# Optimization experiments

Hardware: AMD Instinct MI355X
Metric: run time of the kernel (lower is better)

Reference implementation:

```python
import jax, jax.numpy as jnp
import numpy as np

B, C, H, W, O = 32, 512, 28, 28, 1024


def _make_sketch(key, input_dim, output_dim):
    kh, ks = jax.random.split(key)
    rand_h = jax.random.randint(kh, (input_dim,), 0, output_dim)
    rand_s = jax.random.randint(ks, (input_dim,), 0, 2).astype(jnp.float32) * 2.0 - 1.0
    sketch = jnp.zeros((output_dim, input_dim), dtype=jnp.float32)
    return sketch.at[rand_h, jnp.arange(input_dim)].set(rand_s)


def setup_inputs() -> dict:
    key = jax.random.key(0)
    k1, k2, k3, k4 = jax.random.split(key, 4)
    x1 = jax.random.normal(k1, (B, C, H, W), dtype=jnp.float32)
    x2 = jax.random.normal(k2, (B, C, H, W), dtype=jnp.float32)
    sketch1 = _make_sketch(k3, C, O)
    sketch2 = _make_sketch(k4, C, O)
    return {"x1": x1, "x2": x2, "sketch1": sketch1, "sketch2": sketch2}


def reference(x1, x2, sketch1, sketch2):
    b, c, h, w = x1.shape
    out_dim = sketch1.shape[0]
    # [B, C, H*W] -> [B, N, C]
    x1_flat = x1.reshape(b, c, h * w).transpose(0, 2, 1)
    x2_flat = x2.reshape(b, c, h * w).transpose(0, 2, 1)
    # count-sketch projection via dense matmul (faithful to F.linear)
    proj1 = jnp.einsum('bnc,oc->bno', x1_flat, sketch1)
    proj2 = jnp.einsum('bnc,oc->bno', x2_flat, sketch2)
    orig_dtype = proj1.dtype
    # circular convolution via FFT along output_dim axis
    fft1 = jnp.fft.fft(proj1.astype(jnp.float32), axis=-1)
    fft2 = jnp.fft.fft(proj2.astype(jnp.float32), axis=-1)
    cbp_flat = jnp.fft.ifft(fft1 * fft2, axis=-1).real.astype(orig_dtype)
    # [B, N, O] -> [B, O, H, W]
    return cbp_flat.transpose(0, 2, 1).reshape(b, out_dim, h, w)
```

## Files before the change

### kernel.cpp

```cpp
#include <hip/hip_runtime.h>

#define O_DIM   1024
#define C_DIM   512
#define HW      784
#define B_DIM   32
#define T_POS   8
#define NTILES  (HW / T_POS)
#define NTHREADS 256

__device__ __forceinline__ float2 cmul(float2 a, float2 b) {
    return make_float2(a.x * b.x - a.y * b.y, a.x * b.y + a.y * b.x);
}

template<int SGN>
__device__ __forceinline__ void fft32(float2 y[32]) {
    static constexpr float C32[16] = {
        1.f, 0.98078528f, 0.92387953f, 0.83146961f,
        0.70710678f, 0.55557023f, 0.38268343f, 0.19509032f,
        0.f, -0.19509032f, -0.38268343f, -0.55557023f,
        -0.70710678f, -0.83146961f, -0.92387953f, -0.98078528f};
    static constexpr float S32[16] = {
        0.f, 0.19509032f, 0.38268343f, 0.55557023f,
        0.70710678f, 0.83146961f, 0.92387953f, 0.98078528f,
        1.f, 0.98078528f, 0.92387953f, 0.83146961f,
        0.70710678f, 0.55557023f, 0.38268343f, 0.19509032f};
#pragma unroll
    for (int s = 0; s < 5; ++s) {
        const int L = 32 >> s;
        const int h = 16 >> s;
#pragma unroll
        for (int u = 0; u < 16; ++u) {
            const int blk = u >> (4 - s);
            const int t   = u & (h - 1);
            const int i   = blk * L + t;
            const int m   = t << s;
            float2 a = y[i], b = y[i + h];
            y[i] = make_float2(a.x + b.x, a.y + b.y);
            float2 d = make_float2(a.x - b.x, a.y - b.y);
            if (m == 0) {
                y[i + h] = d;
            } else if (m == 8) {
                y[i + h] = (SGN < 0) ? make_float2(d.y, -d.x)
                                     : make_float2(-d.y, d.x);
            } else {
                float2 w = make_float2(C32[m], (SGN < 0) ? -S32[m] : S32[m]);
                y[i + h] = cmul(d, w);
            }
        }
    }
}

__device__ const int REV5[32] = {
    0,16,8,24,4,20,12,28,2,18,10,26,6,22,14,30,
    1,17,9,25,5,21,13,29,3,19,11,27,7,23,15,31};

template<int SGN>
__device__ __forceinline__ void four_step_core(float2* zg, int p, float2 y[32]) {
#pragma unroll
    for (int n2 = 0; n2 < 32; ++n2)
        y[n2] = zg[p + 32 * n2];
    __builtin_amdgcn_wave_barrier();
    fft32<SGN>(y);
    float sv, cv;
    __sincosf((float)SGN * 6.283185307179586f * (float)p * (1.f / 1024.f), &sv, &cv);
    const float2 stw = make_float2(cv, sv);
    float2 w = make_float2(1.f, 0.f);
#pragma unroll
    for (int k2 = 0; k2 < 32; ++k2) {
        float2 val = y[REV5[k2]];
        if (k2 > 0) val = cmul(val, w);
        zg[k2 * 32 + ((p + k2) & 31)] = val;
        w = cmul(w, stw);
    }
    __builtin_amdgcn_wave_barrier();
#pragma unroll
    for (int n1 = 0; n1 < 32; ++n1)
        y[n1] = zg[p * 32 + ((n1 + p) & 31)];
    __builtin_amdgcn_wave_barrier();
    fft32<SGN>(y);
}

__global__ void extract_sketch(const float* __restrict__ sk1,
                               const float* __restrict__ sk2,
                               int* __restrict__ h, float* __restrict__ s) {
    const int o = blockIdx.x;
    for (int c = threadIdx.x; c < C_DIM; c += blockDim.x) {
        float v1 = sk1[o * C_DIM + c];
        if (v1 != 0.f) { h[c] = o; s[c] = v1; }
        float v2 = sk2[o * C_DIM + c];
        if (v2 != 0.f) { h[C_DIM + c] = o; s[C_DIM + c] = v2; }
    }
}

__global__ __launch_bounds__(NTHREADS, 2)
void cbp_main(const float* __restrict__ x1, const float* __restrict__ x2,
              const int* __restrict__ h1, const int* __restrict__ h2,
              const float* __restrict__ s1, const float* __restrict__ s2,
              float* __restrict__ out) {
    __shared__ float4 LBUF[4096];
    float2 (*Z)[O_DIM] = reinterpret_cast<float2(*)[O_DIM]>(LBUF);
    float*  R = reinterpret_cast<float*>(LBUF);

    const int tid  = threadIdx.x;
    const int b    = blockIdx.x / NTILES;
    const int tile = blockIdx.x % NTILES;
    const int n0   = tile * T_POS;

    const int c0 = tid;
    const int c1 = tid + NTHREADS;
    const int xoff = b * (C_DIM * HW) + n0;
    const float4* p10 = (const float4*)(x1 + xoff + c0 * HW);
    const float4* p11 = (const float4*)(x1 + xoff + c1 * HW);
    const float4* p20 = (const float4*)(x2 + xoff + c0 * HW);
    const float4* p21 = (const float4*)(x2 + xoff + c1 * HW);
    float4 a0 = p10[0], a1 = p10[1];
    float4 b0 = p11[0], b1 = p11[1];
    float4 d0 = p20[0], d1 = p20[1];
    float4 e0 = p21[0], e1 = p21[1];
    const int   q10 = h1[c0], q11 = h1[c1], q20 = h2[c0], q21 = h2[c1];
    const float w10 = s1[c0], w11 = s1[c1], w20 = s2[c0], w21 = s2[c1];

#pragma unroll
    for (int i = 0; i < 4096 / NTHREADS; ++i)
        LBUF[tid + NTHREADS * i] = make_float4(0.f, 0.f, 0.f, 0.f);
    __syncthreads();

    {
        float v[8];
        v[0]=a0.x; v[1]=a0.y; v[2]=a0.z; v[3]=a0.w;
        v[4]=a1.x; v[5]=a1.y; v[6]=a1.z; v[7]=a1.w;
#pragma unroll
        for (int j = 0; j < 8; ++j) atomicAdd(&Z[j][q10].x, w10 * v[j]);
        v[0]=b0.x; v[1]=b0.y; v[2]=b0.z; v[3]=b0.w;
        v[4]=b1.x; v[5]=b1.y; v[6]=b1.z; v[7]=b1.w;
#pragma unroll
        for (int j = 0; j < 8; ++j) atomicAdd(&Z[j][q11].x, w11 * v[j]);
        v[0]=d0.x; v[1]=d0.y; v[2]=d0.z; v[3]=d0.w;
        v[4]=d1.x; v[5]=d1.y; v[6]=d1.z; v[7]=d1.w;
#pragma unroll
        for (int j = 0; j < 8; ++j) atomicAdd(&Z[j][q20].y, w20 * v[j]);
        v[0]=e0.x; v[1]=e0.y; v[2]=e0.z; v[3]=e0.w;
        v[4]=e1.x; v[5]=e1.y; v[6]=e1.z; v[7]=e1.w;
#pragma unroll
        for (int j = 0; j < 8; ++j) atomicAdd(&Z[j][q21].y, w21 * v[j]);
    }
    __syncthreads();

    const int g = tid >> 5;
    const int p = tid & 31;
    float2* zg = &Z[g][0];
    float2 y[32];

    four_step_core<-1>(zg, p, y);
#pragma unroll
    for (int k1 = 0; k1 < 32; ++k1)
        zg[p + 32 * k1] = y[REV5[k1]];
    __builtin_amdgcn_wave_barrier();

#pragma unroll
    for (int m = 0; m < 16; ++m) {
        const int k = p + (m << 5);
        if (k == 0) {
            float2 z0 = zg[0];
            float2 z5 = zg[512];
            zg[0]   = make_float2(z0.x * z0.y, 0.f);
            zg[512] = make_float2(z5.x * z5.y, 0.f);
        } else {
            float2 za = zg[k];
            float2 zb = zg[1024 - k];
            float2 F1 = make_float2(0.5f * (za.x + zb.x), 0.5f * (za.y - zb.y));
            float2 F2 = make_float2(0.5f * (za.y + zb.y), -0.5f * (za.x - zb.x));
            float2 G  = cmul(F1, F2);
            zg[k]        = G;
            zg[1024 - k] = make_float2(G.x, -G.y);
        }
    }
    __builtin_amdgcn_wave_barrier();

    four_step_core<1>(zg, p, y);
    __syncthreads();

#pragma unroll
    for (int k1 = 0; k1 < 32; ++k1)
        R[(p + 32 * k1) * 10 + g] = y[REV5[k1]].x * (1.f / 1024.f);
    __syncthreads();

    const int obase = b * (O_DIM * HW) + n0;
#pragma unroll
    for (int r = 0; r < O_DIM / NTHREADS; ++r) {
        const int o = tid + NTHREADS * r;
        const float* rp = &R[o * 10];
        float4 v0 = make_float4(rp[0], rp[1], rp[2], rp[3]);
        float4 v1 = make_float4(rp[4], rp[5], rp[6], rp[7]);
        float4* dst = (float4*)(out + obase + o * HW);
        dst[0] = v0;
        dst[1] = v1;
    }
}

extern "C" void kernel_launch(void* const* d_in, const int* in_sizes, int n_in,
                              void* d_out, int out_size, void* d_ws, size_t ws_size,
                              hipStream_t stream) {
    const float* x1  = (const float*)d_in[0];
    const float* x2  = (const float*)d_in[1];
    const float* sk1 = (const float*)d_in[2];
    const float* sk2 = (const float*)d_in[3];
    float* out = (float*)d_out;

    int*   h = (int*)d_ws;
    float* s = (float*)((char*)d_ws + 4096);

    hipLaunchKernelGGL(extract_sketch, dim3(O_DIM), dim3(256), 0, stream,
                       sk1, sk2, h, s);
    hipLaunchKernelGGL(cbp_main, dim3(B_DIM * NTILES), dim3(NTHREADS), 0, stream,
                       x1, x2, h, h + C_DIM, s, s + C_DIM, out);
}
```

Baseline: 363.1 us.

## Split each 1024-point FFT across a full wave using permlane32 swaps

Doubles the block to 512 threads so each 64-lane wave handles one position's 1024-point FFT instead of 32 lanes. The first radix-2 stage of each 32-point sub-FFT is done across wave halves with permlane32_swap, leaving 16 points per lane. This halves per-thread register arrays and spreads the scatter-add over one channel per thread, aiming for higher occupancy (launch bounds raised to 4 blocks). The result staging pad is changed from 10 to 11 to reduce LDS bank conflicts. It adds cross-lane traffic and more LDS contention per CU.

```diff
diff --git a/kernel.cpp b/kernel.cpp
--- a/kernel.cpp
+++ b/kernel.cpp
@@ -6,78 +6,103 @@
 #define B_DIM   32
 #define T_POS   8
 #define NTILES  (HW / T_POS)
-#define NTHREADS 256
+#define NTHREADS 512
+#define RPAD    11
 
 __device__ __forceinline__ float2 cmul(float2 a, float2 b) {
     return make_float2(a.x * b.x - a.y * b.y, a.x * b.y + a.y * b.x);
 }
 
+static constexpr float C32T[16] = {
+    1.f, 0.98078528f, 0.92387953f, 0.83146961f,
+    0.70710678f, 0.55557023f, 0.38268343f, 0.19509032f,
+    0.f, -0.19509032f, -0.38268343f, -0.55557023f,
+    -0.70710678f, -0.83146961f, -0.92387953f, -0.98078528f};
+static constexpr float S32T[16] = {
+    0.f, 0.19509032f, 0.38268343f, 0.55557023f,
+    0.70710678f, 0.83146961f, 0.92387953f, 0.98078528f,
+    1.f, 0.98078528f, 0.92387953f, 0.83146961f,
+    0.70710678f, 0.55557023f, 0.38268343f, 0.19509032f};
+static constexpr int REV4[16] = {0,8,4,12,2,10,6,14,1,9,5,13,3,11,7,15};
+
+__device__ __forceinline__ float other_half(float v) {
+    unsigned u = __float_as_uint(v);
+    auto r = __builtin_amdgcn_permlane32_swap(u, u, false, false);
+    return __uint_as_float(((unsigned)r[0]) ^ ((unsigned)r[1]) ^ u);
+}
+
 template<int SGN>
-__device__ __forceinline__ void fft32(float2 y[32]) {
-    static constexpr float C32[16] = {
-        1.f, 0.98078528f, 0.92387953f, 0.83146961f,
-        0.70710678f, 0.55557023f, 0.38268343f, 0.19509032f,
-        0.f, -0.19509032f, -0.38268343f, -0.55557023f,
-        -0.70710678f, -0.83146961f, -0.92387953f, -0.98078528f};
-    static constexpr float S32[16] = {
-        0.f, 0.19509032f, 0.38268343f, 0.55557023f,
-        0.70710678f, 0.83146961f, 0.92387953f, 0.98078528f,
-        1.f, 0.98078528f, 0.92387953f, 0.83146961f,
-        0.70710678f, 0.55557023f, 0.38268343f, 0.19509032f};
-#pragma unroll
-    for (int s = 0; s < 5; ++s) {
-        const int L = 32 >> s;
-        const int h = 16 >> s;
-#pragma unroll
-        for (int u = 0; u < 16; ++u) {
-            const int blk = u >> (4 - s);
-            const int t   = u & (h - 1);
+__device__ __forceinline__ void fft16x(float2 y[16], int h) {
+#pragma unroll
+    for (int j = 0; j < 16; ++j) {
+        float2 own = y[j];
+        float2 oth = make_float2(other_half(own.x), other_half(own.y));
+        float2 s = make_float2(own.x + oth.x, own.y + oth.y);
+        float2 f = make_float2(own.x - oth.x, own.y - oth.y);
+        float2 dd;
+        if (j == 0) {
+            dd = make_float2(-f.x, -f.y);
+        } else if (j == 8) {
+            dd = (SGN < 0) ? make_float2(-f.y, f.x) : make_float2(f.y, -f.x);
+        } else {
+            float2 wn = make_float2(-C32T[j], (SGN < 0) ? S32T[j] : -S32T[j]);
+            dd = cmul(f, wn);
+        }
+        y[j] = h ? dd : s;
+    }
+#pragma unroll
+    for (int s = 0; s < 4; ++s) {
+        const int hh = 8 >> s;
+        const int L  = 16 >> s;
+#pragma unroll
+        for (int u = 0; u < 8; ++u) {
+            const int blk = u >> (3 - s);
+            const int t   = u & (hh - 1);
             const int i   = blk * L + t;
-            const int m   = t << s;
-            float2 a = y[i], b = y[i + h];
+            const int m   = (t << s) * 2;
+            float2 a = y[i], b = y[i + hh];
             y[i] = make_float2(a.x + b.x, a.y + b.y);
             float2 d = make_float2(a.x - b.x, a.y - b.y);
             if (m == 0) {
-                y[i + h] = d;
+                y[i + hh] = d;
             } else if (m == 8) {
-                y[i + h] = (SGN < 0) ? make_float2(d.y, -d.x)
-                                     : make_float2(-d.y, d.x);
+                y[i + hh] = (SGN < 0) ? make_float2(d.y, -d.x)
+                                      : make_float2(-d.y, d.x);
             } else {
-                float2 w = make_float2(C32[m], (SGN < 0) ? -S32[m] : S32[m]);
-                y[i + h] = cmul(d, w);
+                float2 wv = make_float2(C32T[m], (SGN < 0) ? -S32T[m] : S32T[m]);
+                y[i + hh] = cmul(d, wv);
             }
         }
     }
 }
 
-__device__ const int REV5[32] = {
-    0,16,8,24,4,20,12,28,2,18,10,26,6,22,14,30,
-    1,17,9,25,5,21,13,29,3,19,11,27,7,23,15,31};
-
 template<int SGN>
-__device__ __forceinline__ void four_step_core(float2* zg, int p, float2 y[32]) {
-#pragma unroll
-    for (int n2 = 0; n2 < 32; ++n2)
-        y[n2] = zg[p + 32 * n2];
-    __builtin_amdgcn_wave_barrier();
-    fft32<SGN>(y);
-    float sv, cv;
-    __sincosf((float)SGN * 6.283185307179586f * (float)p * (1.f / 1024.f), &sv, &cv);
-    const float2 stw = make_float2(cv, sv);
-    float2 w = make_float2(1.f, 0.f);
-#pragma unroll
-    for (int k2 = 0; k2 < 32; ++k2) {
-        float2 val = y[REV5[k2]];
-        if (k2 > 0) val = cmul(val, w);
-        zg[k2 * 32 + ((p + k2) & 31)] = val;
+__device__ __forceinline__ void wave_fft(float2* zg, int c, int h, float2 y[16]) {
+#pragma unroll
+    for (int j = 0; j < 16; ++j)
+        y[j] = zg[c + 32 * (16 * h + j)];
+    __builtin_amdgcn_wave_barrier();
+    fft16x<SGN>(y, h);
+    float sv, cv, sv2, cv2;
+    __sincosf((float)SGN * 6.283185307179586f * (float)(c * h) * (1.f / 1024.f),
+              &sv, &cv);
+    __sincosf((float)SGN * 6.283185307179586f * (float)(2 * c) * (1.f / 1024.f),
+              &sv2, &cv2);
+    float2 w = make_float2(cv, sv);
+    const float2 stw = make_float2(cv2, sv2);
+#pragma unroll
+    for (int mm = 0; mm < 16; ++mm) {
+        float2 val = cmul(y[REV4[mm]], w);
+        const int k2 = 2 * mm + h;
+        zg[k2 * 32 + ((c + k2) & 31)] = val;
         w = cmul(w, stw);
     }
     __builtin_amdgcn_wave_barrier();
 #pragma unroll
-    for (int n1 = 0; n1 < 32; ++n1)
-        y[n1] = zg[p * 32 + ((n1 + p) & 31)];
-    __builtin_amdgcn_wave_barrier();
-    fft32<SGN>(y);
+    for (int j = 0; j < 16; ++j)
+        y[j] = zg[c * 32 + ((16 * h + j + c) & 31)];
+    __builtin_amdgcn_wave_barrier();
+    fft16x<SGN>(y, h);
 }
 
 __global__ void extract_sketch(const float* __restrict__ sk1,
@@ -92,7 +117,7 @@
     }
 }
 
-__global__ __launch_bounds__(NTHREADS, 2)
+__global__ __launch_bounds__(NTHREADS, 4)
 void cbp_main(const float* __restrict__ x1, const float* __restrict__ x2,
               const int* __restrict__ h1, const int* __restrict__ h2,
               const float* __restrict__ s1, const float* __restrict__ s2,
@@ -106,19 +131,13 @@
     const int tile = blockIdx.x % NTILES;
     const int n0   = tile * T_POS;
 
-    const int c0 = tid;
-    const int c1 = tid + NTHREADS;
-    const int xoff = b * (C_DIM * HW) + n0;
-    const float4* p10 = (const float4*)(x1 + xoff + c0 * HW);
-    const float4* p11 = (const float4*)(x1 + xoff + c1 * HW);
-    const float4* p20 = (const float4*)(x2 + xoff + c0 * HW);
-    const float4* p21 = (const float4*)(x2 + xoff + c1 * HW);
-    float4 a0 = p10[0], a1 = p10[1];
-    float4 b0 = p11[0], b1 = p11[1];
-    float4 d0 = p20[0], d1 = p20[1];
-    float4 e0 = p21[0], e1 = p21[1];
-    const int   q10 = h1[c0], q11 = h1[c1], q20 = h2[c0], q21 = h2[c1];
-    const float w10 = s1[c0], w11 = s1[c1], w20 = s2[c0], w21 = s2[c1];
+    const int c = tid;
+    const float* px1 = x1 + b * (C_DIM * HW) + c * HW + n0;
+    const float* px2 = x2 + b * (C_DIM * HW) + c * HW + n0;
+    float4 a0 = ((const float4*)px1)[0], a1 = ((const float4*)px1)[1];
+    float4 d0 = ((const float4*)px2)[0], d1 = ((const float4*)px2)[1];
+    const int   q1 = h1[c], q2 = h2[c];
+    const float w1 = s1[c], w2 = s2[c];
 
 #pragma unroll
     for (int i = 0; i < 4096 / NTHREADS; ++i)
@@ -126,40 +145,31 @@
     __syncthreads();
 
     {
-        float v[8];
-        v[0]=a0.x; v[1]=a0.y; v[2]=a0.z; v[3]=a0.w;
-        v[4]=a1.x; v[5]=a1.y; v[6]=a1.z; v[7]=a1.w;
-#pragma unroll
-        for (int j = 0; j < 8; ++j) atomicAdd(&Z[j][q10].x, w10 * v[j]);
-        v[0]=b0.x; v[1]=b0.y; v[2]=b0.z; v[3]=b0.w;
-        v[4]=b1.x; v[5]=b1.y; v[6]=b1.z; v[7]=b1.w;
-#pragma unroll
-        for (int j = 0; j < 8; ++j) atomicAdd(&Z[j][q11].x, w11 * v[j]);
-        v[0]=d0.x; v[1]=d0.y; v[2]=d0.z; v[3]=d0.w;
-        v[4]=d1.x; v[5]=d1.y; v[6]=d1.z; v[7]=d1.w;
-#pragma unroll
-        for (int j = 0; j < 8; ++j) atomicAdd(&Z[j][q20].y, w20 * v[j]);
-        v[0]=e0.x; v[1]=e0.y; v[2]=e0.z; v[3]=e0.w;
-        v[4]=e1.x; v[5]=e1.y; v[6]=e1.z; v[7]=e1.w;
-#pragma unroll
-        for (int j = 0; j < 8; ++j) atomicAdd(&Z[j][q21].y, w21 * v[j]);
-    }
-    __syncthreads();
-
-    const int g = tid >> 5;
-    const int p = tid & 31;
-    float2* zg = &Z[g][0];
-    float2 y[32];
-
-    four_step_core<-1>(zg, p, y);
-#pragma unroll
-    for (int k1 = 0; k1 < 32; ++k1)
-        zg[p + 32 * k1] = y[REV5[k1]];
-    __builtin_amdgcn_wave_barrier();
-
-#pragma unroll
-    for (int m = 0; m < 16; ++m) {
-        const int k = p + (m << 5);
+        float v[8] = {a0.x, a0.y, a0.z, a0.w, a1.x, a1.y, a1.z, a1.w};
+#pragma unroll
+        for (int j = 0; j < 8; ++j) atomicAdd(&Z[j][q1].x, w1 * v[j]);
+        float u[8] = {d0.x, d0.y, d0.z, d0.w, d1.x, d1.y, d1.z, d1.w};
+#pragma unroll
+        for (int j = 0; j < 8; ++j) atomicAdd(&Z[j][q2].y, w2 * u[j]);
+    }
+    __syncthreads();
+
+    const int wv   = tid >> 6;
+    const int lane = tid & 63;
+    const int cc   = lane & 31;
+    const int hh   = lane >> 5;
+    float2* zg = &Z[wv][0];
+    float2 y[16];
+
+    wave_fft<-1>(zg, cc, hh, y);
+#pragma unroll
+    for (int mm = 0; mm < 16; ++mm)
+        zg[cc + 32 * (2 * mm + hh)] = y[REV4[mm]];
+    __builtin_amdgcn_wave_barrier();
+
+#pragma unroll
+    for (int m = 0; m < 8; ++m) {
+        const int k = lane + (m << 6);
         if (k == 0) {
             float2 z0 = zg[0];
             float2 z5 = zg[512];
@@ -177,19 +187,19 @@
     }
     __builtin_amdgcn_wave_barrier();
 
-    four_step_core<1>(zg, p, y);
-    __syncthreads();
-
-#pragma unroll
-    for (int k1 = 0; k1 < 32; ++k1)
-        R[(p + 32 * k1) * 10 + g] = y[REV5[k1]].x * (1.f / 1024.f);
+    wave_fft<1>(zg, cc, hh, y);
+    __syncthreads();
+
+#pragma unroll
+    for (int mm = 0; mm < 16; ++mm)
+        R[(cc + 32 * (2 * mm + hh)) * RPAD + wv] = y[REV4[mm]].x * (1.f / 1024.f);
     __syncthreads();
 
     const int obase = b * (O_DIM * HW) + n0;
 #pragma unroll
     for (int r = 0; r < O_DIM / NTHREADS; ++r) {
         const int o = tid + NTHREADS * r;
-        const float* rp = &R[o * 10];
+        const float* rp = &R[o * RPAD];
         float4 v0 = make_float4(rp[0], rp[1], rp[2], rp[3]);
         float4 v1 = make_float4(rp[4], rp[5], rp[6], rp[7]);
         float4* dst = (float4*)(out + obase + o * HW);
```

Result: slower. 383.6 us (+5.6%).

## Do spectral product in registers via ds_bpermute and split twiddle recurrence

Applied to the files above, without the earlier changes.

After the forward FFT, the spectrum is no longer written back to LDS and re-read for the pointwise product. Each lane instead fetches its mirror element k and 1024-k from the partner lane with ds_bpermute and computes the product in registers, then feeds the result directly into the inverse FFT. The twiddle recurrence is split into four independent chains seeded with stw^8, stw^16 and stw^24, which shortens the dependency chain, and REV5 becomes a constexpr so indexing resolves at compile time. The cost is higher register pressure from the extra gg[32] array, which could hurt occupancy under launch_bounds(256,2).

```diff
diff --git a/kernel.cpp b/kernel.cpp
--- a/kernel.cpp
+++ b/kernel.cpp
@@ -11,6 +11,10 @@
 __device__ __forceinline__ float2 cmul(float2 a, float2 b) {
     return make_float2(a.x * b.x - a.y * b.y, a.x * b.y + a.y * b.x);
 }
+
+static constexpr int REV5[32] = {
+    0,16,8,24,4,20,12,28,2,18,10,26,6,22,14,30,
+    1,17,9,25,5,21,13,29,3,19,11,27,7,23,15,31};
 
 template<int SGN>
 __device__ __forceinline__ void fft32(float2 y[32]) {
@@ -50,27 +54,36 @@
     }
 }
 
-__device__ const int REV5[32] = {
-    0,16,8,24,4,20,12,28,2,18,10,26,6,22,14,30,
-    1,17,9,25,5,21,13,29,3,19,11,27,7,23,15,31};
-
 template<int SGN>
-__device__ __forceinline__ void four_step_core(float2* zg, int p, float2 y[32]) {
-#pragma unroll
-    for (int n2 = 0; n2 < 32; ++n2)
-        y[n2] = zg[p + 32 * n2];
-    __builtin_amdgcn_wave_barrier();
-    fft32<SGN>(y);
+__device__ __forceinline__ void four_step_B(float2* zg, int p, float2 y[32]) {
     float sv, cv;
     __sincosf((float)SGN * 6.283185307179586f * (float)p * (1.f / 1024.f), &sv, &cv);
     const float2 stw = make_float2(cv, sv);
-    float2 w = make_float2(1.f, 0.f);
-#pragma unroll
-    for (int k2 = 0; k2 < 32; ++k2) {
-        float2 val = y[REV5[k2]];
-        if (k2 > 0) val = cmul(val, w);
-        zg[k2 * 32 + ((p + k2) & 31)] = val;
-        w = cmul(w, stw);
+    float2 t2  = cmul(stw, stw);
+    float2 t4  = cmul(t2, t2);
+    float2 s8  = cmul(t4, t4);
+    float2 s16 = cmul(s8, s8);
+    float2 s24 = cmul(s16, s8);
+    float2 wq0 = make_float2(1.f, 0.f), wq1 = s8, wq2 = s16, wq3 = s24;
+#pragma unroll
+    for (int m = 0; m < 8; ++m) {
+        {   const int k2 = m;
+            float2 val = y[REV5[k2]];
+            if (k2 > 0) val = cmul(val, wq0);
+            zg[k2 * 32 + ((p + k2) & 31)] = val; }
+        {   const int k2 = 8 + m;
+            float2 val = cmul(y[REV5[k2]], wq1);
+            zg[k2 * 32 + ((p + k2) & 31)] = val; }
+        {   const int k2 = 16 + m;
+            float2 val = cmul(y[REV5[k2]], wq2);
+            zg[k2 * 32 + ((p + k2) & 31)] = val; }
+        {   const int k2 = 24 + m;
+            float2 val = cmul(y[REV5[k2]], wq3);
+            zg[k2 * 32 + ((p + k2) & 31)] = val; }
+        if (m < 7) {
+            wq0 = cmul(wq0, stw); wq1 = cmul(wq1, stw);
+            wq2 = cmul(wq2, stw); wq3 = cmul(wq3, stw);
+        }
     }
     __builtin_amdgcn_wave_barrier();
 #pragma unroll
@@ -146,43 +159,45 @@
     }
     __syncthreads();
 
-    const int g = tid >> 5;
-    const int p = tid & 31;
+    const int g    = tid >> 5;
+    const int p    = tid & 31;
+    const int lane = tid & 63;
     float2* zg = &Z[g][0];
     float2 y[32];
 
-    four_step_core<-1>(zg, p, y);
+#pragma unroll
+    for (int n2 = 0; n2 < 32; ++n2)
+        y[n2] = zg[p + 32 * n2];
+    __builtin_amdgcn_wave_barrier();
+    fft32<-1>(y);
+    four_step_B<-1>(zg, p, y);
+
+    const int paddr = (((lane & 32) | ((32 - p) & 31))) << 2;
+    float2 gg[32];
+#pragma unroll
+    for (int n2 = 0; n2 < 32; ++n2) {
+        float2 za = y[REV5[n2]];
+        float2 yb = y[REV5[31 - n2]];
+        float2 zb;
+        zb.x = __uint_as_float((unsigned)__builtin_amdgcn_ds_bpermute(
+                   paddr, (int)__float_as_uint(yb.x)));
+        zb.y = __uint_as_float((unsigned)__builtin_amdgcn_ds_bpermute(
+                   paddr, (int)__float_as_uint(yb.y)));
+        float2 self = y[REV5[(32 - n2) & 31]];
+        zb.x = (p == 0) ? self.x : zb.x;
+        zb.y = (p == 0) ? self.y : zb.y;
+        float2 F1 = make_float2(0.5f * (za.x + zb.x), 0.5f * (za.y - zb.y));
+        float2 F2 = make_float2(0.5f * (za.y + zb.y), -0.5f * (za.x - zb.x));
+        gg[n2] = cmul(F1, F2);
+    }
+
+    fft32<1>(gg);
+    four_step_B<1>(zg, p, gg);
+    __syncthreads();
+
 #pragma unroll
     for (int k1 = 0; k1 < 32; ++k1)
-        zg[p + 32 * k1] = y[REV5[k1]];
-    __builtin_amdgcn_wave_barrier();
-
-#pragma unroll
-    for (int m = 0; m < 16; ++m) {
-        const int k = p + (m << 5);
-        if (k == 0) {
-            float2 z0 = zg[0];
-            float2 z5 = zg[512];
-            zg[0]   = make_float2(z0.x * z0.y, 0.f);
-            zg[512] = make_float2(z5.x * z5.y, 0.f);
-        } else {
-            float2 za = zg[k];
-            float2 zb = zg[1024 - k];
-            float2 F1 = make_float2(0.5f * (za.x + zb.x), 0.5f * (za.y - zb.y));
-            float2 F2 = make_float2(0.5f * (za.y + zb.y), -0.5f * (za.x - zb.x));
-            float2 G  = cmul(F1, F2);
-            zg[k]        = G;
-            zg[1024 - k] = make_float2(G.x, -G.y);
-        }
-    }
-    __builtin_amdgcn_wave_barrier();
-
-    four_step_core<1>(zg, p, y);
-    __syncthreads();
-
-#pragma unroll
-    for (int k1 = 0; k1 < 32; ++k1)
-        R[(p + 32 * k1) * 10 + g] = y[REV5[k1]].x * (1.f / 1024.f);
+        R[(p + 32 * k1) * 10 + g] = gg[REV5[k1]].x * (1.f / 1024.f);
     __syncthreads();
 
     const int obase = b * (O_DIM * HW) + n0;
```

Result: no change. 359.1 us (-1.1%).
